# Kernel tuning notes

Hardware: AMD Instinct MI355X
Metric: run time of the kernel (lower is better)

The kernel has to match this reference:

```python
import jax, jax.numpy as jnp
import numpy as np

B, T, K = 64, 2000, 256
BLANK_LOGPROB = -1.0
NEG = jnp.float32(-1e30)  # stand-in for -inf, safe under logaddexp


def setup_inputs() -> dict:
    key = jax.random.key(0)
    k1, k2, k3 = jax.random.split(key, 3)
    attn_logprob = jax.random.normal(k1, (B, 1, T, K), dtype=jnp.float32)
    key_lens = jax.random.randint(k2, (B,), K // 2, K + 1)
    query_lens = jax.random.randint(k3, (B,), T // 2, T + 1)
    return {"attn_logprob": attn_logprob, "key_lens": key_lens, "query_lens": query_lens}


def _forward_sum(attn_logprob, key_lens, query_lens):
    # attn_logprob: [B, 1, T, K]; targets are 1..K_b (strictly increasing, all distinct)
    Bn, _, Tn, Kn = attn_logprob.shape
    logp = attn_logprob[:, 0]                                   # [B, T, K]
    # pad blank class at key index 0 (torch F.pad(pad=(1,0), value=blank_logprob))
    padded = jnp.pad(logp, ((0, 0), (0, 0), (1, 0)), constant_values=BLANK_LOGPROB)  # [B,T,K+1]
    # masked log_softmax over classes 0..K_b (matches per-sample slice [:key_lens+1])
    key_idx = jnp.arange(Kn + 1)
    key_mask = key_idx[None, :] <= key_lens[:, None]            # [B, K+1]
    masked = jnp.where(key_mask[:, None, :], padded, NEG)
    log_probs = jax.nn.log_softmax(masked, axis=-1)             # [B, T, K+1]

    # CTC forward DP. States s = 0..2K: even -> blank (class 0), odd -> label (s+1)//2.
    S = 2 * Kn + 1
    s_idx = jnp.arange(S)
    lab = jnp.where(s_idx % 2 == 0, 0, (s_idx + 1) // 2)        # class index per state
    # skip transition s-2 -> s allowed for odd s >= 3 (all labels distinct)
    skip_ok = (s_idx % 2 == 1) & (s_idx >= 3)

    emit0 = log_probs[:, 0, :][:, lab]                          # [B, S]
    alpha0 = jnp.full((Bn, S), NEG, dtype=log_probs.dtype)
    alpha0 = alpha0.at[:, 0].set(emit0[:, 0]).at[:, 1].set(emit0[:, 1])

    xs = jnp.moveaxis(log_probs[:, 1:, :], 1, 0)                # [T-1, B, K+1]
    ts = jnp.arange(1, Tn)

    def step(alpha, inp):
        x, t = inp
        emit = x[:, lab]                                        # [B, S]
        sh1 = jnp.concatenate([jnp.full((Bn, 1), NEG, alpha.dtype), alpha[:, :-1]], axis=1)
        sh2 = jnp.concatenate([jnp.full((Bn, 2), NEG, alpha.dtype), alpha[:, :-2]], axis=1)
        sh2 = jnp.where(skip_ok[None, :], sh2, NEG)
        new = jnp.logaddexp(jnp.logaddexp(alpha, sh1), sh2) + emit
        # freeze alpha once t >= query_lens[b] so final carry = alpha at t = T_b - 1
        return jnp.where((t < query_lens)[:, None], new, alpha), None

    alpha_final, _ = jax.lax.scan(step, alpha0, (xs, ts))       # [B, S]

    last = 2 * key_lens                                          # final state index per sample
    a_last = jnp.take_along_axis(alpha_final, last[:, None], axis=1)[:, 0]
    a_prev = jnp.take_along_axis(alpha_final, (last - 1)[:, None], axis=1)[:, 0]
    nll = -jnp.logaddexp(a_last, a_prev)                         # per-sample CTC NLL
    # torch CTCLoss(reduction='mean') on a batch of 1: divide by target length
    loss = nll / jnp.maximum(key_lens, 1).astype(nll.dtype)
    loss = jnp.where(nll > 0.5e30, 0.0, loss)                    # zero_infinity
    return jnp.mean(loss)


def reference(attn_logprob, key_lens, query_lens):
    return _forward_sum(attn_logprob, key_lens, query_lens)
```

## Files before the change

kernel.cpp:

```cpp
#include <hip/hip_runtime.h>
#include <cstdint>
#include <cstddef>

#define BB    64
#define TB    2000
#define KB    256
#define WPB   125
#define RPW   16
#define NLSEB 2000

constexpr float LOG2E = 1.4426950408889634f;
constexpr float LN2f  = 0.6931471805599453f;
constexpr float WBF   = 0.36787944117144233f;

__device__ __forceinline__ float exp2i(int k) {
  return __uint_as_float((uint32_t)(127 + k) << 23);
}
__device__ __forceinline__ float shr1z(float v) {
  return __int_as_float(__builtin_amdgcn_update_dpp(
      0, __float_as_int(v), 0x138, 0xF, 0xF, true));
}
__device__ __forceinline__ float dmax64(float v) {
#define DSTEP(ctrl, rm, bc)                                                  \
  { float t = __int_as_float(__builtin_amdgcn_update_dpp(                    \
        __float_as_int(v), __float_as_int(v), (ctrl), (rm), 0xF, (bc)));     \
    v = fmaxf(v, t); }
  DSTEP(0x111, 0xF, true) DSTEP(0x112, 0xF, true) DSTEP(0x114, 0xF, true)
  DSTEP(0x118, 0xF, true) DSTEP(0x142, 0xA, false) DSTEP(0x143, 0xC, false)
#undef DSTEP
  return __int_as_float(__builtin_amdgcn_readlane(__float_as_int(v), 63));
}
__device__ __forceinline__ float dsum64(float v) {
#define DSTEP(ctrl, rm, bc)                                                  \
  { float t = __int_as_float(__builtin_amdgcn_update_dpp(                    \
        __float_as_int(v), __float_as_int(v), (ctrl), (rm), 0xF, (bc)));     \
    v += t; }
  DSTEP(0x111, 0xF, true) DSTEP(0x112, 0xF, true) DSTEP(0x114, 0xF, true)
  DSTEP(0x118, 0xF, true) DSTEP(0x142, 0xA, false) DSTEP(0x143, 0xC, false)
#undef DSTEP
  return v;
}
__device__ __forceinline__ float wsum64(float v) {
#pragma unroll
  for (int m = 32; m >= 1; m >>= 1) v += __shfl_xor(v, m, 64);
  return v;
}

typedef const __attribute__((address_space(1))) unsigned int* gas1p;
typedef __attribute__((address_space(3))) unsigned int* las3p;

__global__ __launch_bounds__(256, 1)
void fsl_main(const float* __restrict__ x, const int* __restrict__ key_lens,
              const int* __restrict__ query_lens, float* __restrict__ partial,
              float* __restrict__ alast, float* __restrict__ aprev) {
  __shared__ __align__(16) char ring[86016];
  __shared__ __align__(16) int prodG[4];
  __shared__ int consG;

  const int tid  = threadIdx.x;
  const int lane = tid & 63;
  const int w    = tid >> 6;

  if (blockIdx.x < BB) {
    const int b    = blockIdx.x;
    const int kl   = key_lens[b];
    const int qlen = query_lens[b];
    const int total = qlen - 1;
    const int ng    = (total + 7) >> 3;
    const float* xb  = x + (size_t)b * (TB * KB);
    const char*  xbc = (const char*)xb;
    const int lane16 = lane << 4;

    if (tid == 0) { prodG[0] = 0; prodG[1] = 0; prodG[2] = 0; prodG[3] = 0x7fffffff; consG = 0; }
    __syncthreads();

    if (w == 0) {
      float a0 = 0.f, a1 = 0.f, a2 = 0.f, a3 = 0.f;
      float b0 = 0.f, b1 = 0.f, b2 = 0.f, b3 = 0.f, s512 = 0.f;
      if (lane == 0) { a0 = WBF; b0 = __builtin_amdgcn_exp2f(xb[0] * LOG2E); }
      int Cw = 0;
      float m_red = dmax64(fmaxf(a0, b0));

      float4 e0, e1, e2, e3, e4, e5, e6, e7;
      float4 f0, f1, f2, f3, f4, f5, f6, f7;
      float4 g0, g1, g2, g3, g4, g5, g6, g7;

#define POLL(GN) do {                                                        \
    const int tgt_ = (GN);                                                   \
    for (;;) {                                                               \
      __asm__ __volatile__("" ::: "memory");                                 \
      const int4 fl_ = *(const int4*)prodG;                                  \
      if (min(fl_.x, min(fl_.y, fl_.z)) >= tgt_) break;                      \
    }                                                                        \
    __asm__ __volatile__("" ::: "memory");                                   \
  } while (0)

#define LD8(E, g) do {                                                       \
    const char* sb_ = ring + (((g) & 7) << 13) + lane16;                     \
    E##0 = *(const float4*)(sb_);                                            \
    E##1 = *(const float4*)(sb_ + 1024);                                     \
    E##2 = *(const float4*)(sb_ + 2048);                                     \
    E##3 = *(const float4*)(sb_ + 3072);                                     \
    E##4 = *(const float4*)(sb_ + 4096);                                     \
    E##5 = *(const float4*)(sb_ + 5120);                                     \
    E##6 = *(const float4*)(sb_ + 6144);                                     \
    E##7 = *(const float4*)(sb_ + 7168);                                     \
  } while (0)

#define STEP1(EV) do {                                                       \
    const float pm1 = shr1z(b3);                                             \
    const float t0_ = a0 + pm1;                                              \
    const float t1_ = a1 + b0;                                               \
    const float t2_ = a2 + b1;                                               \
    const float t3_ = a3 + b2;                                               \
    s512 = s512 + b3;                                                        \
    b0 = (b0 + t0_) * EV.x;                                                  \
    b1 = (b1 + t1_) * EV.y;                                                  \
    b2 = (b2 + t2_) * EV.z;                                                  \
    b3 = (b3 + t3_) * EV.w;                                                  \
    a0 = t0_; a1 = t1_; a2 = t2_; a3 = t3_;                                  \
  } while (0)

#define STEP1G(EV, J) do { if ((J) < rem_) { STEP1(EV); } } while (0)

#define RUN8(E)  do { STEP1(E##0); STEP1(E##1); STEP1(E##2); STEP1(E##3);    \
                      STEP1(E##4); STEP1(E##5); STEP1(E##6); STEP1(E##7); } while (0)
#define RUN8G(E, RM) do { const int rem_ = (RM);                             \
                      STEP1G(E##0,0); STEP1G(E##1,1); STEP1G(E##2,2);        \
                      STEP1G(E##3,3); STEP1G(E##4,4); STEP1G(E##5,5);        \
                      STEP1G(E##6,6); STEP1G(E##7,7); } while (0)

#define APPLY() do {                                                         \
    int e_ = (int)((__float_as_uint(m_red) >> 23) & 0xFF) - 127;             \
    if (!(m_red > 0.f)) e_ = -24;                                            \
    const int k_ = e_ + 24;                      \
    if (k_ > 126) {                                                          \
      const int kh_ = k_ >> 1;                                               \
      const float s1_ = exp2i(-kh_), s2_ = exp2i(-(k_ - kh_));               \
      a0 *= s1_; a1 *= s1_; a2 *= s1_; a3 *= s1_;                            \
      b0 *= s1_; b1 *= s1_; b2 *= s1_; b3 *= s1_; s512 *= s1_;               \
      a0 *= s2_; a1 *= s2_; a2 *= s2_; a3 *= s2_;                            \
      b0 *= s2_; b1 *= s2_; b2 *= s2_; b3 *= s2_; s512 *= s2_;               \
    } else {                                                                 \
      const float s_ = exp2i(-k_);                                           \
      a0 *= s_; a1 *= s_; a2 *= s_; a3 *= s_;                                \
      b0 *= s_; b1 *= s_; b2 *= s_; b3 *= s_; s512 *= s_;                    \
    }                                                                        \
    Cw += k_;                                                                \
  } while (0)

#define MEASURE() do {                                                       \
    float ml_ = fmaxf(fmaxf(fmaxf(a0, a1), fmaxf(a2, a3)),                   \
                      fmaxf(fmaxf(b0, b1), fmaxf(b2, b3)));                  \
    ml_ = fmaxf(ml_, s512);                                                  \
    m_red = dmax64(ml_);                                                     \
  } while (0)

#define RUNGRP(E, G) do {                                                    \
    if (8 * (G) + 8 <= total) { RUN8(E); }                                   \
    else { RUN8G(E, total - 8 * (G)); }                                      \
    APPLY(); MEASURE();                                                      \
  } while (0)

      POLL(3);
      LD8(e, 0);
      if (1 < ng) LD8(f, 1);
      if (2 < ng) LD8(g, 2);
      int cg = 0;
      while (cg + 6 <= ng && 8 * (cg + 3) <= total) {
        POLL(cg + 6);
        RUN8(e); APPLY(); MEASURE(); LD8(e, cg + 3);
        RUN8(f); APPLY(); MEASURE(); LD8(f, cg + 4);
        RUN8(g); APPLY(); MEASURE(); LD8(g, cg + 5);
        __asm__ __volatile__("" ::: "memory");
        if (lane == 0) *(volatile int*)&consG = cg + 6;
        cg += 3;
      }
      for (; cg < ng; cg += 3) {
        POLL(min(cg + 6, ng));
        RUNGRP(e, cg);
        if (cg + 3 < ng) LD8(e, cg + 3);
        if (cg + 1 < ng) {
          RUNGRP(f, cg + 1);
          if (cg + 4 < ng) LD8(f, cg + 4);
        }
        if (cg + 2 < ng) {
          RUNGRP(g, cg + 2);
          if (cg + 5 < ng) LD8(g, cg + 5);
        }
        __asm__ __volatile__("" ::: "memory");
        if (lane == 0) *(volatile int*)&consG = cg + 6;
      }
#undef POLL
#undef LD8
#undef STEP1
#undef STEP1G
#undef RUN8
#undef RUN8G
#undef APPLY
#undef MEASURE
#undef RUNGRP

      float* ev = (float*)ring;
      float* od = (float*)(ring + 4096);
      *(float4*)(ev + (lane << 2)) = make_float4(a0, a1, a2, a3);
      *(float4*)(od + (lane << 2)) = make_float4(b0, b1, b2, b3);
      if (lane == 63) *(float*)(ring + 8192) = s512;
      __asm__ __volatile__("" ::: "memory");
      if (lane == 0) {
        const float aL = (kl < 256) ? ev[kl] : *(float*)(ring + 8192);
        const float aP = od[kl - 1];
        const float dC = (float)Cw - (float)total * LOG2E;
        alast[b] = (log2f(aL) + dC) * LN2f;
        aprev[b] = (log2f(aP) + dC) * LN2f;
      }
    } else {
      const int pw = w - 1;
      const int c0 = lane << 2;
      const float bs0 = (c0 + 0 < kl) ? LOG2E : -20000.f;
      const float bs1 = (c0 + 1 < kl) ? LOG2E : -20000.f;
      const float bs2 = (c0 + 2 < kl) ? LOG2E : -20000.f;
      const float bs3 = (c0 + 3 < kl) ? LOG2E : -20000.f;
      volatile int* vc = &consG;

      float4 A0, A1, A2, A3, A4, A5, A6, A7;
      float4 B0, B1, B2, B3, B4, B5, B6, B7;
      float4 C0, C1, C2, C3, C4, C5, C6, C7;

#define LOADG(P, GG) do {                                                    \
    const int rb_ = 8 * (GG) + 1;                                            \
    P##0 = *(const float4*)(xbc + (size_t)min(rb_ + 0, TB - 1) * 1024 + lane16); \
    P##1 = *(const float4*)(xbc + (size_t)min(rb_ + 1, TB - 1) * 1024 + lane16); \
    P##2 = *(const float4*)(xbc + (size_t)min(rb_ + 2, TB - 1) * 1024 + lane16); \
    P##3 = *(const float4*)(xbc + (size_t)min(rb_ + 3, TB - 1) * 1024 + lane16); \
    P##4 = *(const float4*)(xbc + (size_t)min(rb_ + 4, TB - 1) * 1024 + lane16); \
    P##5 = *(const float4*)(xbc + (size_t)min(rb_ + 5, TB - 1) * 1024 + lane16); \
    P##6 = *(const float4*)(xbc + (size_t)min(rb_ + 6, TB - 1) * 1024 + lane16); \
    P##7 = *(const float4*)(xbc + (size_t)min(rb_ + 7, TB - 1) * 1024 + lane16); \
  } while (0)

#define PR1(V, J) do {                                                       \
    float4 wv_;                                                              \
    wv_.x = __builtin_amdgcn_exp2f(fmaf(V.x, LOG2E, bs0));                   \
    wv_.y = __builtin_amdgcn_exp2f(fmaf(V.y, LOG2E, bs1));                   \
    wv_.z = __builtin_amdgcn_exp2f(fmaf(V.z, LOG2E, bs2));                   \
    wv_.w = __builtin_amdgcn_exp2f(fmaf(V.w, LOG2E, bs3));                   \
    *(float4*)(dstb_ + ((J) << 10)) = wv_;                                   \
  } while (0)

#define PROC(P, GG) do {                                                     \
    if ((GG) >= 8) {                                    \
      int c_ = *vc;                                                          \
      while (c_ < (GG) - 7) { __builtin_amdgcn_s_sleep(2); c_ = *vc; }       \
      __asm__ __volatile__("" ::: "memory");                                 \
    }                                                                        \
    char* dstb_ = ring + (((GG) & 7) << 13) + lane16;                        \
    PR1(P##0, 0); PR1(P##1, 1); PR1(P##2, 2); PR1(P##3, 3);                  \
    PR1(P##4, 4); PR1(P##5, 5); PR1(P##6, 6); PR1(P##7, 7);                  \
    __asm__ __volatile__("s_waitcnt lgkmcnt(0)" ::: "memory");               \
    if (lane == 0) *(volatile int*)&prodG[pw] = (GG) + 3;                    \
  } while (0)

      LOADG(A, pw); LOADG(B, pw + 3);
      int g = pw;
      for (;;) {
        LOADG(C, g + 6);
        PROC(A, g);
        g += 3; if (g >= ng) break;
        LOADG(A, g + 6);
        PROC(B, g);
        g += 3; if (g >= ng) break;
        LOADG(B, g + 6);
        PROC(C, g);
        g += 3; if (g >= ng) break;
      }
#undef LOADG
#undef PR1
#undef PROC
      __asm__ __volatile__("" ::: "memory");
      if (lane == 0) *(volatile int*)&prodG[pw] = 0x7fffffff;
    }

  } else {
    const int gwid = (blockIdx.x - BB) * 4 + w;
    const int b    = gwid / WPB;
    const int widx = gwid - b * WPB;
    const int kl   = key_lens[b];
    const int qlen = query_lens[b];
    const float* xb = x + (size_t)b * (TB * KB);
    const int c0 = lane * 4;
    const float bA = (c0 + 0 < kl) ? 0.f : -20000.f;
    const float bBv= (c0 + 1 < kl) ? 0.f : -20000.f;
    const float bC = (c0 + 2 < kl) ? 0.f : -20000.f;
    const float bD = (c0 + 3 < kl) ? 0.f : -20000.f;
    float acc = 0.f;
    const int tbase = widx * RPW;
#pragma unroll 4
    for (int k = 0; k < RPW; ++k) {
      const int t = tbase + k;
      const float4 v = *(const float4*)(xb + (size_t)t * KB + c0);
      float s = __builtin_amdgcn_exp2f(fmaf(v.x, LOG2E, bA))
              + __builtin_amdgcn_exp2f(fmaf(v.y, LOG2E, bBv))
              + __builtin_amdgcn_exp2f(fmaf(v.z, LOG2E, bC))
              + __builtin_amdgcn_exp2f(fmaf(v.w, LOG2E, bD));
      s = dsum64(s);
      s += WBF;
      const float l2 = __builtin_amdgcn_logf(s);
      acc += (t < qlen) ? l2 : 0.f;
    }
    if (lane == 63) partial[gwid] = acc * LN2f;
  }
}

__global__ __launch_bounds__(256)
void fsl_finish(const float* __restrict__ partial, const int* __restrict__ key_lens,
                const float* __restrict__ alast, const float* __restrict__ aprev,
                float* __restrict__ out) {
  const int tid = threadIdx.x;
  const int b = tid >> 2, q = tid & 3;
  float s = 0.f;
  for (int j = q; j < WPB; j += 4) s += partial[b * WPB + j];
  s += __shfl_xor(s, 1, 64);
  s += __shfl_xor(s, 2, 64);
  float lossb = 0.f;
  if (q == 0) {
    const float SumLse = s;
    const float al = alast[b], ap = aprev[b];
    const float mx = fmaxf(al, ap);
    const float lae = (mx == -INFINITY) ? -INFINITY
                                        : mx + log1pf(expf(-fabsf(al - ap)));
    const float nll = SumLse - lae;
    const int kl = key_lens[b];
    float lv = nll / (float)max(kl, 1);
    if (nll > 5e29f) lv = 0.f;
    lossb = lv;
  }
  float v = wsum64(lossb);
  __shared__ float sm[4];
  if ((tid & 63) == 0) sm[tid >> 6] = v;
  __syncthreads();
  if (tid == 0) out[0] = ((sm[0] + sm[1]) + (sm[2] + sm[3])) * (1.0f / 64.0f);
}

extern "C" void kernel_launch(void* const* d_in, const int* in_sizes, int n_in,
                              void* d_out, int out_size, void* d_ws, size_t ws_size,
                              hipStream_t stream) {
  const float* x     = (const float*)d_in[0];
  const int*   klens = (const int*)d_in[1];
  const int*   qlens = (const int*)d_in[2];
  float* out = (float*)d_out;

  float* partial = (float*)d_ws;
  float* alast   = partial + BB * WPB;
  float* aprev   = alast + BB;

  fsl_main  <<<BB + NLSEB, 256, 0, stream>>>(x, klens, qlens, partial, alast, aprev);
  fsl_finish<<<1, 256, 0, stream>>>(partial, klens, alast, aprev, out);
}
```

Measured before the change: 121.1 us.

## Process two batch samples per scan block with interleaved recurrences

Each scan block now runs the CTC alpha recurrence for two samples at once, interleaving their independent dependency chains in one wavefront to hide latency. Each sample gets its own LDS ring, and the producer waves load and exponentiate both. This halves the number of scan blocks. The pipeline depth and the load prefetch pattern change: the consumer keeps two groups in flight instead of three, and producers double-buffer instead of triple-buffer. The log-sum-exp path now issues all 16 row loads up front. Risks are higher register pressure, the shallower pipeline, and a per-block time set by the longer of the two sequences.

Result: slower. 221.5 us (+83.0%).

```diff
diff --git a/kernel.cpp b/kernel.cpp
--- a/kernel.cpp
+++ b/kernel.cpp
@@ -5,6 +5,7 @@
 #define BB    64
 #define TB    2000
 #define KB    256
+#define NSCB  32
 #define WPB   125
 #define RPW   16
 #define NLSEB 2000
@@ -46,14 +47,11 @@
   return v;
 }
 
-typedef const __attribute__((address_space(1))) unsigned int* gas1p;
-typedef __attribute__((address_space(3))) unsigned int* las3p;
-
 __global__ __launch_bounds__(256, 1)
 void fsl_main(const float* __restrict__ x, const int* __restrict__ key_lens,
               const int* __restrict__ query_lens, float* __restrict__ partial,
               float* __restrict__ alast, float* __restrict__ aprev) {
-  __shared__ __align__(16) char ring[86016];
+  __shared__ __align__(16) char ring2[131072];
   __shared__ __align__(16) int prodG[4];
   __shared__ int consG;
 
@@ -61,29 +59,23 @@
   const int lane = tid & 63;
   const int w    = tid >> 6;
 
-  if (blockIdx.x < BB) {
-    const int b    = blockIdx.x;
-    const int kl   = key_lens[b];
-    const int qlen = query_lens[b];
-    const int total = qlen - 1;
-    const int ng    = (total + 7) >> 3;
-    const float* xb  = x + (size_t)b * (TB * KB);
-    const char*  xbc = (const char*)xb;
+  if (blockIdx.x < NSCB) {
+    const int bA = blockIdx.x * 2;
+    const int bB = bA + 1;
+    const int klA = key_lens[bA], klB = key_lens[bB];
+    const int qA = query_lens[bA], qB = query_lens[bB];
+    const int totA = qA - 1, totB = qB - 1;
+    const int ngA = (totA + 7) >> 3, ngB = (totB + 7) >> 3;
+    const int NG = max(ngA, ngB);
+    const char* xbcA = (const char*)(x + (size_t)bA * (TB * KB));
+    const char* xbcB = (const char*)(x + (size_t)bB * (TB * KB));
     const int lane16 = lane << 4;
-
-    if (tid == 0) { prodG[0] = 0; prodG[1] = 0; prodG[2] = 0; prodG[3] = 0x7fffffff; consG = 0; }
+    char* const ringA = ring2;
+    char* const ringB = ring2 + 65536;
+
+    if (tid == 0) { prodG[0] = 0; prodG[1] = 0; prodG[2] = 0;
+                    prodG[3] = 0x7fffffff; consG = 0; }
     __syncthreads();
-
-    if (w == 0) {
-      float a0 = 0.f, a1 = 0.f, a2 = 0.f, a3 = 0.f;
-      float b0 = 0.f, b1 = 0.f, b2 = 0.f, b3 = 0.f, s512 = 0.f;
-      if (lane == 0) { a0 = WBF; b0 = __builtin_amdgcn_exp2f(xb[0] * LOG2E); }
-      int Cw = 0;
-      float m_red = dmax64(fmaxf(a0, b0));
-
-      float4 e0, e1, e2, e3, e4, e5, e6, e7;
-      float4 f0, f1, f2, f3, f4, f5, f6, f7;
-      float4 g0, g1, g2, g3, g4, g5, g6, g7;
 
 #define POLL(GN) do {                                                        \
     const int tgt_ = (GN);                                                   \
@@ -95,8 +87,8 @@
     __asm__ __volatile__("" ::: "memory");                                   \
   } while (0)
 
-#define LD8(E, g) do {                                                       \
-    const char* sb_ = ring + (((g) & 7) << 13) + lane16;                     \
+#define LD8(E, g, RING) do {                                                 \
+    const char* sb_ = (RING) + (((g) & 7) << 13) + lane16;                   \
     E##0 = *(const float4*)(sb_);                                            \
     E##1 = *(const float4*)(sb_ + 1024);                                     \
     E##2 = *(const float4*)(sb_ + 2048);                                     \
@@ -107,7 +99,25 @@
     E##7 = *(const float4*)(sb_ + 7168);                                     \
   } while (0)
 
-#define STEP1(EV) do {                                                       \
+    if (w == 0) {
+      float aA0 = 0.f, aA1 = 0.f, aA2 = 0.f, aA3 = 0.f;
+      float bA0 = 0.f, bA1 = 0.f, bA2 = 0.f, bA3 = 0.f, sA512 = 0.f;
+      float aB0 = 0.f, aB1 = 0.f, aB2 = 0.f, aB3 = 0.f;
+      float bB0 = 0.f, bB1 = 0.f, bB2 = 0.f, bB3 = 0.f, sB512 = 0.f;
+      if (lane == 0) {
+        aA0 = WBF; bA0 = __builtin_amdgcn_exp2f(((const float*)xbcA)[0] * LOG2E);
+        aB0 = WBF; bB0 = __builtin_amdgcn_exp2f(((const float*)xbcB)[0] * LOG2E);
+      }
+      int CwA = 0, CwB = 0;
+      float mrA = dmax64(fmaxf(aA0, bA0));
+      float mrB = dmax64(fmaxf(aB0, bB0));
+
+      float4 eA0, eA1, eA2, eA3, eA4, eA5, eA6, eA7;
+      float4 fA0, fA1, fA2, fA3, fA4, fA5, fA6, fA7;
+      float4 eB0, eB1, eB2, eB3, eB4, eB5, eB6, eB7;
+      float4 fB0, fB1, fB2, fB3, fB4, fB5, fB6, fB7;
+
+#define STEP1N(EV, a0,a1,a2,a3, b0,b1,b2,b3, s512) do {                      \
     const float pm1 = shr1z(b3);                                             \
     const float t0_ = a0 + pm1;                                              \
     const float t1_ = a1 + b0;                                               \
@@ -120,19 +130,35 @@
     b3 = (b3 + t3_) * EV.w;                                                  \
     a0 = t0_; a1 = t1_; a2 = t2_; a3 = t3_;                                  \
   } while (0)
-
-#define STEP1G(EV, J) do { if ((J) < rem_) { STEP1(EV); } } while (0)
-
-#define RUN8(E)  do { STEP1(E##0); STEP1(E##1); STEP1(E##2); STEP1(E##3);    \
-                      STEP1(E##4); STEP1(E##5); STEP1(E##6); STEP1(E##7); } while (0)
-#define RUN8G(E, RM) do { const int rem_ = (RM);                             \
-                      STEP1G(E##0,0); STEP1G(E##1,1); STEP1G(E##2,2);        \
-                      STEP1G(E##3,3); STEP1G(E##4,4); STEP1G(E##5,5);        \
-                      STEP1G(E##6,6); STEP1G(E##7,7); } while (0)
-
-#define APPLY() do {                                                         \
-    int e_ = (int)((__float_as_uint(m_red) >> 23) & 0xFF) - 127;             \
-    if (!(m_red > 0.f)) e_ = -24;                                            \
+#define STEPA(EV) STEP1N(EV, aA0,aA1,aA2,aA3, bA0,bA1,bA2,bA3, sA512)
+#define STEPB(EV) STEP1N(EV, aB0,aB1,aB2,aB3, bB0,bB1,bB2,bB3, sB512)
+
+#define STEPP(EA, EB) do { STEPA(EA); STEPB(EB); } while (0)
+#define RUN8P(PA, PB) do {                                                   \
+    STEPP(PA##0, PB##0); STEPP(PA##1, PB##1);                                \
+    STEPP(PA##2, PB##2); STEPP(PA##3, PB##3);                                \
+    STEPP(PA##4, PB##4); STEPP(PA##5, PB##5);                                \
+    STEPP(PA##6, PB##6); STEPP(PA##7, PB##7);                                \
+  } while (0)
+
+#define RUN8A(E) do { STEPA(E##0); STEPA(E##1); STEPA(E##2); STEPA(E##3);    \
+                      STEPA(E##4); STEPA(E##5); STEPA(E##6); STEPA(E##7); } while (0)
+#define RUN8B(E) do { STEPB(E##0); STEPB(E##1); STEPB(E##2); STEPB(E##3);    \
+                      STEPB(E##4); STEPB(E##5); STEPB(E##6); STEPB(E##7); } while (0)
+#define RUN8GA(E, RM) do { const int rem_ = (RM);                            \
+    if (0 < rem_) STEPA(E##0); if (1 < rem_) STEPA(E##1);                    \
+    if (2 < rem_) STEPA(E##2); if (3 < rem_) STEPA(E##3);                    \
+    if (4 < rem_) STEPA(E##4); if (5 < rem_) STEPA(E##5);                    \
+    if (6 < rem_) STEPA(E##6); if (7 < rem_) STEPA(E##7); } while (0)
+#define RUN8GB(E, RM) do { const int rem_ = (RM);                            \
+    if (0 < rem_) STEPB(E##0); if (1 < rem_) STEPB(E##1);                    \
+    if (2 < rem_) STEPB(E##2); if (3 < rem_) STEPB(E##3);                    \
+    if (4 < rem_) STEPB(E##4); if (5 < rem_) STEPB(E##5);                    \
+    if (6 < rem_) STEPB(E##6); if (7 < rem_) STEPB(E##7); } while (0)
+
+#define APPLYN(mr, Cw, a0,a1,a2,a3, b0,b1,b2,b3, s512) do {                  \
+    int e_ = (int)((__float_as_uint(mr) >> 23) & 0xFF) - 127;                \
+    if (!((mr) > 0.f)) e_ = -24;                                             \
     const int k_ = e_ + 24;                      \
     if (k_ > 126) {                                                          \
       const int kh_ = k_ >> 1;                                               \
@@ -148,141 +174,182 @@
     }                                                                        \
     Cw += k_;                                                                \
   } while (0)
-
-#define MEASURE() do {                                                       \
+#define MEASN(mr, a0,a1,a2,a3, b0,b1,b2,b3, s512) do {                       \
     float ml_ = fmaxf(fmaxf(fmaxf(a0, a1), fmaxf(a2, a3)),                   \
                       fmaxf(fmaxf(b0, b1), fmaxf(b2, b3)));                  \
     ml_ = fmaxf(ml_, s512);                                                  \
-    m_red = dmax64(ml_);                                                     \
-  } while (0)
-
-#define RUNGRP(E, G) do {                                                    \
-    if (8 * (G) + 8 <= total) { RUN8(E); }                                   \
-    else { RUN8G(E, total - 8 * (G)); }                                      \
-    APPLY(); MEASURE();                                                      \
+    mr = dmax64(ml_);                                                        \
+  } while (0)
+#define APPLYA() APPLYN(mrA, CwA, aA0,aA1,aA2,aA3, bA0,bA1,bA2,bA3, sA512)
+#define APPLYB() APPLYN(mrB, CwB, aB0,aB1,aB2,aB3, bB0,bB1,bB2,bB3, sB512)
+#define MEASA()  MEASN(mrA, aA0,aA1,aA2,aA3, bA0,bA1,bA2,bA3, sA512)
+#define MEASB()  MEASN(mrB, aB0,aB1,aB2,aB3, bB0,bB1,bB2,bB3, sB512)
+
+#define GRP(PA, PB, G) do {                                                  \
+    const bool fA_ = (8 * (G) + 8 <= totA), fB_ = (8 * (G) + 8 <= totB);     \
+    if (fA_ && fB_) { RUN8P(PA, PB); }                                       \
+    else {                                                                   \
+      if (fA_) { RUN8A(PA); }                                                \
+      else if (8 * (G) < totA) { RUN8GA(PA, totA - 8 * (G)); }               \
+      if (fB_) { RUN8B(PB); }                                                \
+      else if (8 * (G) < totB) { RUN8GB(PB, totB - 8 * (G)); }               \
+    }                                                                        \
+    APPLYA(); MEASA(); APPLYB(); MEASB();                                    \
   } while (0)
 
       POLL(3);
-      LD8(e, 0);
-      if (1 < ng) LD8(f, 1);
-      if (2 < ng) LD8(g, 2);
-      int cg = 0;
-      while (cg + 6 <= ng && 8 * (cg + 3) <= total) {
-        POLL(cg + 6);
-        RUN8(e); APPLY(); MEASURE(); LD8(e, cg + 3);
-        RUN8(f); APPLY(); MEASURE(); LD8(f, cg + 4);
-        RUN8(g); APPLY(); MEASURE(); LD8(g, cg + 5);
+      LD8(eA, 0, ringA); LD8(eB, 0, ringB);
+      LD8(fA, 1, ringA); LD8(fB, 1, ringB);
+      int g = 0;
+      for (;;) {
+        POLL(min(g + 3, NG));
+        GRP(eA, eB, g);
+        if (g + 2 < NG) { LD8(eA, g + 2, ringA); LD8(eB, g + 2, ringB); }
         __asm__ __volatile__("" ::: "memory");
-        if (lane == 0) *(volatile int*)&consG = cg + 6;
-        cg += 3;
+        if (lane == 0) *(volatile int*)&consG = g + 3;
+        if (++g >= NG) break;
+        POLL(min(g + 3, NG));
+        GRP(fA, fB, g);
+        if (g + 2 < NG) { LD8(fA, g + 2, ringA); LD8(fB, g + 2, ringB); }
+        __asm__ __volatile__("" ::: "memory");
+        if (lane == 0) *(volatile int*)&consG = g + 3;
+        if (++g >= NG) break;
       }
-      for (; cg < ng; cg += 3) {
-        POLL(min(cg + 6, ng));
-        RUNGRP(e, cg);
-        if (cg + 3 < ng) LD8(e, cg + 3);
-        if (cg + 1 < ng) {
-          RUNGRP(f, cg + 1);
-          if (cg + 4 < ng) LD8(f, cg + 4);
-        }
-        if (cg + 2 < ng) {
-          RUNGRP(g, cg + 2);
-          if (cg + 5 < ng) LD8(g, cg + 5);
-        }
-        __asm__ __volatile__("" ::: "memory");
-        if (lane == 0) *(volatile int*)&consG = cg + 6;
-      }
-#undef POLL
-#undef LD8
-#undef STEP1
-#undef STEP1G
-#undef RUN8
-#undef RUN8G
-#undef APPLY
-#undef MEASURE
-#undef RUNGRP
-
-      float* ev = (float*)ring;
-      float* od = (float*)(ring + 4096);
-      *(float4*)(ev + (lane << 2)) = make_float4(a0, a1, a2, a3);
-      *(float4*)(od + (lane << 2)) = make_float4(b0, b1, b2, b3);
-      if (lane == 63) *(float*)(ring + 8192) = s512;
+#undef STEP1N
+#undef STEPA
+#undef STEPB
+#undef STEPP
+#undef RUN8P
+#undef RUN8A
+#undef RUN8B
+#undef RUN8GA
+#undef RUN8GB
+#undef APPLYN
+#undef MEASN
+#undef APPLYA
+#undef APPLYB
+#undef MEASA
+#undef MEASB
+#undef GRP
+
+      *(float4*)((float*)ringA + (lane << 2)) = make_float4(aA0, aA1, aA2, aA3);
+      *(float4*)((float*)(ringA + 4096) + (lane << 2)) = make_float4(bA0, bA1, bA2, bA3);
+      if (lane == 63) *(float*)(ringA + 8192) = sA512;
+      *(float4*)((float*)ringB + (lane << 2)) = make_float4(aB0, aB1, aB2, aB3);
+      *(float4*)((float*)(ringB + 4096) + (lane << 2)) = make_float4(bB0, bB1, bB2, bB3);
+      if (lane == 63) *(float*)(ringB + 8192) = sB512;
       __asm__ __volatile__("" ::: "memory");
       if (lane == 0) {
-        const float aL = (kl < 256) ? ev[kl] : *(float*)(ring + 8192);
-        const float aP = od[kl - 1];
-        const float dC = (float)Cw - (float)total * LOG2E;
-        alast[b] = (log2f(aL) + dC) * LN2f;
-        aprev[b] = (log2f(aP) + dC) * LN2f;
+        const float aLA = (klA < 256) ? ((const float*)ringA)[klA]
+                                      : *(const float*)(ringA + 8192);
+        const float aPA = ((const float*)(ringA + 4096))[klA - 1];
+        const float dCA = (float)CwA - (float)totA * LOG2E;
+        alast[bA] = (log2f(aLA) + dCA) * LN2f;
+        aprev[bA] = (log2f(aPA) + dCA) * LN2f;
+        const float aLB = (klB < 256) ? ((const float*)ringB)[klB]
+                                      : *(const float*)(ringB + 8192);
+        const float aPB = ((const float*)(ringB + 4096))[klB - 1];
+        const float dCB = (float)CwB - (float)totB * LOG2E;
+        alast[bB] = (log2f(aLB) + dCB) * LN2f;
+        aprev[bB] = (log2f(aPB) + dCB) * LN2f;
       }
     } else {
       const int pw = w - 1;
       const int c0 = lane << 2;
-      const float bs0 = (c0 + 0 < kl) ? LOG2E : -20000.f;
-      const float bs1 = (c0 + 1 < kl) ? LOG2E : -20000.f;
-      const float bs2 = (c0 + 2 < kl) ? LOG2E : -20000.f;
-      const float bs3 = (c0 + 3 < kl) ? LOG2E : -20000.f;
+      const float bsA0 = (c0 + 0 < klA) ? LOG2E : -20000.f;
+      const float bsA1 = (c0 + 1 < klA) ? LOG2E : -20000.f;
+      const float bsA2 = (c0 + 2 < klA) ? LOG2E : -20000.f;
+      const float bsA3 = (c0 + 3 < klA) ? LOG2E : -20000.f;
+      const float bsB0 = (c0 + 0 < klB) ? LOG2E : -20000.f;
+      const float bsB1 = (c0 + 1 < klB) ? LOG2E : -20000.f;
+      const float bsB2 = (c0 + 2 < klB) ? LOG2E : -20000.f;
+      const float bsB3 = (c0 + 3 < klB) ? LOG2E : -20000.f;
       volatile int* vc = &consG;
 
-      float4 A0, A1, A2, A3, A4, A5, A6, A7;
-      float4 B0, B1, B2, B3, B4, B5, B6, B7;
-      float4 C0, C1, C2, C3, C4, C5, C6, C7;
-
-#define LOADG(P, GG) do {                                                    \
+      float4 XA0, XA1, XA2, XA3, XA4, XA5, XA6, XA7;
+      float4 XB0, XB1, XB2, XB3, XB4, XB5, XB6, XB7;
+      float4 YA0, YA1, YA2, YA3, YA4, YA5, YA6, YA7;
+      float4 YB0, YB1, YB2, YB3, YB4, YB5, YB6, YB7;
+
+#define LOADG2(PA, PB, GG) do {                                              \
     const int rb_ = 8 * (GG) + 1;                                            \
-    P##0 = *(const float4*)(xbc + (size_t)min(rb_ + 0, TB - 1) * 1024 + lane16); \
-    P##1 = *(const float4*)(xbc + (size_t)min(rb_ + 1, TB - 1) * 1024 + lane16); \
-    P##2 = *(const float4*)(xbc + (size_t)min(rb_ + 2, TB - 1) * 1024 + lane16); \
-    P##3 = *(const float4*)(xbc + (size_t)min(rb_ + 3, TB - 1) * 1024 + lane16); \
-    P##4 = *(const float4*)(xbc + (size_t)min(rb_ + 4, TB - 1) * 1024 + lane16); \
-    P##5 = *(const float4*)(xbc + (size_t)min(rb_ + 5, TB - 1) * 1024 + lane16); \
-    P##6 = *(const float4*)(xbc + (size_t)min(rb_ + 6, TB - 1) * 1024 + lane16); \
-    P##7 = *(const float4*)(xbc + (size_t)min(rb_ + 7, TB - 1) * 1024 + lane16); \
-  } while (0)
-
-#define PR1(V, J) do {                                                       \
+    PA##0 = *(const float4*)(xbcA + (size_t)min(rb_ + 0, TB - 1) * 1024 + lane16); \
+    PA##1 = *(const float4*)(xbcA + (size_t)min(rb_ + 1, TB - 1) * 1024 + lane16); \
+    PA##2 = *(const float4*)(xbcA + (size_t)min(rb_ + 2, TB - 1) * 1024 + lane16); \
+    PA##3 = *(const float4*)(xbcA + (size_t)min(rb_ + 3, TB - 1) * 1024 + lane16); \
+    PA##4 = *(const float4*)(xbcA + (size_t)min(rb_ + 4, TB - 1) * 1024 + lane16); \
+    PA##5 = *(const float4*)(xbcA + (size_t)min(rb_ + 5, TB - 1) * 1024 + lane16); \
+    PA##6 = *(const float4*)(xbcA + (size_t)min(rb_ + 6, TB - 1) * 1024 + lane16); \
+    PA##7 = *(const float4*)(xbcA + (size_t)min(rb_ + 7, TB - 1) * 1024 + lane16); \
+    PB##0 = *(const float4*)(xbcB + (size_t)min(rb_ + 0, TB - 1) * 1024 + lane16); \
+    PB##1 = *(const float4*)(xbcB + (size_t)min(rb_ + 1, TB - 1) * 1024 + lane16); \
+    PB##2 = *(const float4*)(xbcB + (size_t)min(rb_ + 2, TB - 1) * 1024 + lane16); \
+    PB##3 = *(const float4*)(xbcB + (size_t)min(rb_ + 3, TB - 1) * 1024 + lane16); \
+    PB##4 = *(const float4*)(xbcB + (size_t)min(rb_ + 4, TB - 1) * 1024 + lane16); \
+    PB##5 = *(const float4*)(xbcB + (size_t)min(rb_ + 5, TB - 1) * 1024 + lane16); \
+    PB##6 = *(const float4*)(xbcB + (size_t)min(rb_ + 6, TB - 1) * 1024 + lane16); \
+    PB##7 = *(const float4*)(xbcB + (size_t)min(rb_ + 7, TB - 1) * 1024 + lane16); \
+  } while (0)
+
+#define PR1M(V, J, M0, M1, M2, M3, DST) do {                                 \
     float4 wv_;                                                              \
-    wv_.x = __builtin_amdgcn_exp2f(fmaf(V.x, LOG2E, bs0));                   \
-    wv_.y = __builtin_amdgcn_exp2f(fmaf(V.y, LOG2E, bs1));                   \
-    wv_.z = __builtin_amdgcn_exp2f(fmaf(V.z, LOG2E, bs2));                   \
-    wv_.w = __builtin_amdgcn_exp2f(fmaf(V.w, LOG2E, bs3));                   \
-    *(float4*)(dstb_ + ((J) << 10)) = wv_;                                   \
-  } while (0)
-
-#define PROC(P, GG) do {                                                     \
+    wv_.x = __builtin_amdgcn_exp2f(fmaf(V.x, LOG2E, M0));                    \
+    wv_.y = __builtin_amdgcn_exp2f(fmaf(V.y, LOG2E, M1));                    \
+    wv_.z = __builtin_amdgcn_exp2f(fmaf(V.z, LOG2E, M2));                    \
+    wv_.w = __builtin_amdgcn_exp2f(fmaf(V.w, LOG2E, M3));                    \
+    *(float4*)((DST) + ((J) << 10)) = wv_;                                   \
+  } while (0)
+
+#define PROC2(PA, PB, GG) do {                                               \
     if ((GG) >= 8) {                                    \
       int c_ = *vc;                                                          \
       while (c_ < (GG) - 7) { __builtin_amdgcn_s_sleep(2); c_ = *vc; }       \
       __asm__ __volatile__("" ::: "memory");                                 \
     }                                                                        \
-    char* dstb_ = ring + (((GG) & 7) << 13) + lane16;                        \
-    PR1(P##0, 0); PR1(P##1, 1); PR1(P##2, 2); PR1(P##3, 3);                  \
-    PR1(P##4, 4); PR1(P##5, 5); PR1(P##6, 6); PR1(P##7, 7);                  \
+    char* dA_ = ringA + (((GG) & 7) << 13) + lane16;                         \
+    char* dB_ = ringB + (((GG) & 7) << 13) + lane16;                         \
+    PR1M(PA##0, 0, bsA0, bsA1, bsA2, bsA3, dA_);                             \
+    PR1M(PA##1, 1, bsA0, bsA1, bsA2, bsA3, dA_);                             \
+    PR1M(PA##2, 2, bsA0, bsA1, bsA2, bsA3, dA_);                             \
+    PR1M(PA##3, 3, bsA0, bsA1, bsA2, bsA3, dA_);                             \
+    PR1M(PA##4, 4, bsA0, bsA1, bsA2, bsA3, dA_);                             \
+    PR1M(PA##5, 5, bsA0, bsA1, bsA2, bsA3, dA_);                             \
+    PR1M(PA##6, 6, bsA0, bsA1, bsA2, bsA3, dA_);                             \
+    PR1M(PA##7, 7, bsA0, bsA1, bsA2, bsA3, dA_);                             \
+    PR1M(PB##0, 0, bsB0, bsB1, bsB2, bsB3, dB_);                             \
+    PR1M(PB##1, 1, bsB0, bsB1, bsB2, bsB3, dB_);                             \
+    PR1M(PB##2, 2, bsB0, bsB1, bsB2, bsB3, dB_);                             \
+    PR1M(PB##3, 3, bsB0, bsB1, bsB2, bsB3, dB_);                             \
+    PR1M(PB##4, 4, bsB0, bsB1, bsB2, bsB3, dB_);                             \
+    PR1M(PB##5, 5, bsB0, bsB1, bsB2, bsB3, dB_);                             \
+    PR1M(PB##6, 6, bsB0, bsB1, bsB2, bsB3, dB_);                             \
+    PR1M(PB##7, 7, bsB0, bsB1, bsB2, bsB3, dB_);                             \
     __asm__ __volatile__("s_waitcnt lgkmcnt(0)" ::: "memory");               \
     if (lane == 0) *(volatile int*)&prodG[pw] = (GG) + 3;                    \
   } while (0)
 
-      LOADG(A, pw); LOADG(B, pw + 3);
+      LOADG2(XA, XB, pw);
+      LOADG2(YA, YB, pw + 3);
       int g = pw;
       for (;;) {
-        LOADG(C, g + 6);
-        PROC(A, g);
-        g += 3; if (g >= ng) break;
-        LOADG(A, g + 6);
-        PROC(B, g);
-        g += 3; if (g >= ng) break;
-        LOADG(B, g + 6);
-        PROC(C, g);
-        g += 3; if (g >= ng) break;
+        PROC2(XA, XB, g);
+        g += 3; if (g >= NG) break;
+        if (g + 3 < NG) LOADG2(XA, XB, g + 3);
+        PROC2(YA, YB, g);
+        g += 3; if (g >= NG) break;
+        if (g + 3 < NG) LOADG2(YA, YB, g + 3);
       }
-#undef LOADG
-#undef PR1
-#undef PROC
+#undef LOADG2
+#undef PR1M
+#undef PROC2
       __asm__ __volatile__("" ::: "memory");
       if (lane == 0) *(volatile int*)&prodG[pw] = 0x7fffffff;
     }
+#undef POLL
+#undef LD8
 
   } else {
-    const int gwid = (blockIdx.x - BB) * 4 + w;
+    const int gwid = (blockIdx.x - NSCB) * 4 + w;
     const int b    = gwid / WPB;
     const int widx = gwid - b * WPB;
     const int kl   = key_lens[b];
@@ -293,21 +360,29 @@
     const float bBv= (c0 + 1 < kl) ? 0.f : -20000.f;
     const float bC = (c0 + 2 < kl) ? 0.f : -20000.f;
     const float bD = (c0 + 3 < kl) ? 0.f : -20000.f;
+    const int tbase = widx * RPW;
+#define LSELOAD(k) const float4 v##k =                                       \
+    *(const float4*)(xb + (size_t)(tbase + (k)) * KB + c0);
+    LSELOAD(0)  LSELOAD(1)  LSELOAD(2)  LSELOAD(3)
+    LSELOAD(4)  LSELOAD(5)  LSELOAD(6)  LSELOAD(7)
+    LSELOAD(8)  LSELOAD(9)  LSELOAD(10) LSELOAD(11)
+    LSELOAD(12) LSELOAD(13) LSELOAD(14) LSELOAD(15)
+#undef LSELOAD
     float acc = 0.f;
-    const int tbase = widx * RPW;
-#pragma unroll 4
-    for (int k = 0; k < RPW; ++k) {
-      const int t = tbase + k;
-      const float4 v = *(const float4*)(xb + (size_t)t * KB + c0);
-      float s = __builtin_amdgcn_exp2f(fmaf(v.x, LOG2E, bA))
-              + __builtin_amdgcn_exp2f(fmaf(v.y, LOG2E, bBv))
-              + __builtin_amdgcn_exp2f(fmaf(v.z, LOG2E, bC))
-              + __builtin_amdgcn_exp2f(fmaf(v.w, LOG2E, bD));
-      s = dsum64(s);
-      s += WBF;
-      const float l2 = __builtin_amdgcn_logf(s);
-      acc += (t < qlen) ? l2 : 0.f;
-    }
+#define LSEROW(k) do {                                                       \
+    float s = __builtin_amdgcn_exp2f(fmaf(v##k.x, LOG2E, bA))                \
+            + __builtin_amdgcn_exp2f(fmaf(v##k.y, LOG2E, bBv))               \
+            + __builtin_amdgcn_exp2f(fmaf(v##k.z, LOG2E, bC))                \
+            + __builtin_amdgcn_exp2f(fmaf(v##k.w, LOG2E, bD));               \
+    s = dsum64(s);                                                           \
+    s += WBF;                                                                \
+    acc += ((tbase + (k)) < qlen) ? __builtin_amdgcn_logf(s) : 0.f;          \
+  } while (0)
+    LSEROW(0);  LSEROW(1);  LSEROW(2);  LSEROW(3);
+    LSEROW(4);  LSEROW(5);  LSEROW(6);  LSEROW(7);
+    LSEROW(8);  LSEROW(9);  LSEROW(10); LSEROW(11);
+    LSEROW(12); LSEROW(13); LSEROW(14); LSEROW(15);
+#undef LSEROW
     if (lane == 63) partial[gwid] = acc * LN2f;
   }
 }
@@ -354,6 +429,6 @@
   float* alast   = partial + BB * WPB;
   float* aprev   = alast + BB;
 
-  fsl_main  <<<BB + NLSEB, 256, 0, stream>>>(x, klens, qlens, partial, alast, aprev);
+  fsl_main  <<<NSCB + NLSEB, 256, 0, stream>>>(x, klens, qlens, partial, alast, aprev);
   fsl_finish<<<1, 256, 0, stream>>>(partial, klens, alast, aprev, out);
 }
```
